# Performance work log

Hardware: AMD Instinct MI355X
Metric: run time of the kernel (lower is better)

The kernel has to match this reference:

```python
import jax, jax.numpy as jnp
import numpy as np

D_MODEL, H, D_K = 768, 12, 64
B, S = 2, 2048
NEG = -1.0e9


def setup_inputs() -> dict:
    key = jax.random.key(0)
    ks = jax.random.split(key, 7)
    q = jax.random.normal(ks[0], (B, S, D_MODEL), dtype=jnp.float32)
    k = jax.random.normal(ks[1], (B, S, D_MODEL), dtype=jnp.float32)
    v = jax.random.normal(ks[2], (B, S, D_MODEL), dtype=jnp.float32)
    mask = jnp.tril(jnp.ones((S, S), dtype=jnp.int32))[None, None]  # [1,1,S,S] causal
    sc = 1.0 / np.sqrt(D_MODEL)
    w_q = jax.random.normal(ks[3], (D_MODEL, D_MODEL), dtype=jnp.float32) * sc
    w_k = jax.random.normal(ks[4], (D_MODEL, D_MODEL), dtype=jnp.float32) * sc
    w_v = jax.random.normal(ks[5], (D_MODEL, D_MODEL), dtype=jnp.float32) * sc
    w_o = jax.random.normal(ks[6], (D_MODEL, D_MODEL), dtype=jnp.float32) * sc
    return {"q": q, "k": k, "v": v, "mask": mask,
            "w_q": w_q, "w_k": w_k, "w_v": w_v, "w_o": w_o}


def reference(q, k, v, mask, w_q, w_k, w_v, w_o):
    # nn.Linear(x) = x @ W.T ; split heads: [B,S,D] -> [B,H,S,Dk]
    def split_heads(x, w):
        y = jnp.einsum('bsd,ed->bse', x, w)
        return y.reshape(x.shape[0], x.shape[1], H, D_K).transpose(0, 2, 1, 3)

    qh = split_heads(q, w_q)
    kh = split_heads(k, w_k)
    vh = split_heads(v, w_v)
    scores = jnp.einsum('bhqd,bhkd->bhqk', qh, kh) / jnp.sqrt(jnp.float32(D_K))
    scores = jnp.where(mask == 0, jnp.float32(NEG), scores)
    attn = jax.nn.softmax(scores, axis=-1)  # dropout p=0 -> identity
    ctx = jnp.einsum('bhqk,bhkd->bhqd', attn, vh)
    ctx = ctx.transpose(0, 2, 1, 3).reshape(q.shape[0], q.shape[1], D_MODEL)
    return jnp.einsum('bsd,ed->bse', ctx, w_o)
```

## Files before the change

kernel.cpp:

```cpp
#include <hip/hip_runtime.h>

#define DM   768
#define HN   12
#define DKH  64
#define BSZ  2
#define SEQ  2048
#define MROWS (BSZ*SEQ)
#define NEGBIG -1.0e9f
#define NSLOT 40
#define QSCALE 0.18033688011112042f

typedef __bf16 bf16;
typedef __bf16 bf16x8 __attribute__((ext_vector_type(8)));
typedef __bf16 bf16x4 __attribute__((ext_vector_type(4)));
typedef float  f32x4  __attribute__((ext_vector_type(4)));
typedef unsigned int uint32;

__device__ __forceinline__ void gload_lds16(const void* g, void* l) {
    __builtin_amdgcn_global_load_lds(
        (const __attribute__((address_space(1))) char*)g,
        (__attribute__((address_space(3))) char*)l, 16, 0, 0);
}

__global__ __launch_bounds__(256) void cvt4(const float* __restrict__ a, const float* __restrict__ b,
                                            const float* __restrict__ c, const float* __restrict__ e,
                                            bf16* __restrict__ x, bf16* __restrict__ y,
                                            bf16* __restrict__ z, bf16* __restrict__ u, int n) {
    const float* s; bf16* d;
    if      (blockIdx.y == 0) { s = a; d = x; }
    else if (blockIdx.y == 1) { s = b; d = y; }
    else if (blockIdx.y == 2) { s = c; d = z; }
    else                      { s = e; d = u; }
    int i = (blockIdx.x * 256 + threadIdx.x) * 4;
    if (i + 3 < n) {
        float4 v = *(const float4*)(s + i);
        bf16x4 o; o[0] = (bf16)v.x; o[1] = (bf16)v.y; o[2] = (bf16)v.z; o[3] = (bf16)v.w;
        *(bf16x4*)(d + i) = o;
    }
}

__global__ __launch_bounds__(256) void gemm_qkv(
    const float* __restrict__ xq, const float* __restrict__ xk, const float* __restrict__ xv,
    const bf16* __restrict__ wq, const bf16* __restrict__ wk, const bf16* __restrict__ wv,
    bf16* __restrict__ qh, bf16* __restrict__ kh, bf16* __restrict__ vt)
{
    __shared__ float Asf[128 * 32];
    __shared__ bf16  Bs[128 * 32];

    const float* A; const bf16* Bw; bf16* Out; float qs;
    if      (blockIdx.z == 0) { A = xq; Bw = wq; Out = qh; qs = QSCALE; }
    else if (blockIdx.z == 1) { A = xk; Bw = wk; Out = kh; qs = 1.0f; }
    else                      { A = xv; Bw = wv; Out = vt; qs = 1.0f; }
    const bool vout = (blockIdx.z == 2);

    const int t = threadIdx.x, w = t >> 6, lane = t & 63;
    const int g = lane >> 4, lo = lane & 15;
    const int mt = blockIdx.x * 128, nt = blockIdx.y * 128;
    const int wr = (w >> 1) * 64, wc = (w & 1) * 64;

    f32x4 acc[4][4] = {};

    for (int k0 = 0; k0 < DM; k0 += 32) {
        #pragma unroll
        for (int i = 0; i < 4; i++) {
            int c = i * 256 + t;
            int row = c >> 3, cc = (c & 7) ^ (row & 7);
            gload_lds16(A + (size_t)(mt + row) * DM + k0 + cc * 4, (char*)Asf + c * 16);
        }
        #pragma unroll
        for (int i = 0; i < 2; i++) {
            int c = i * 256 + t;
            int row = c >> 2, col = (c & 3) * 8;
            gload_lds16(Bw + (size_t)(nt + row) * DM + k0 + col, (char*)Bs + c * 16);
        }
        asm volatile("s_waitcnt vmcnt(0)" ::: "memory");
        __syncthreads();

        bf16x8 af[4], bfr[4];
        #pragma unroll
        for (int m = 0; m < 4; m++) {
            int row = wr + m * 16 + lo;
            const char* rp = (const char*)Asf + row * 128;
            float4 f0 = *(const float4*)(rp + (((2 * g)     ^ (lo & 7)) << 4));
            float4 f1 = *(const float4*)(rp + (((2 * g + 1) ^ (lo & 7)) << 4));
            bf16x8 a;
            a[0] = (bf16)f0.x; a[1] = (bf16)f0.y; a[2] = (bf16)f0.z; a[3] = (bf16)f0.w;
            a[4] = (bf16)f1.x; a[5] = (bf16)f1.y; a[6] = (bf16)f1.z; a[7] = (bf16)f1.w;
            af[m] = a;
        }
        #pragma unroll
        for (int n = 0; n < 4; n++)
            bfr[n] = *(const bf16x8*)&Bs[(wc + n * 16 + lo) * 32 + g * 8];
        #pragma unroll
        for (int m = 0; m < 4; m++)
            #pragma unroll
            for (int n = 0; n < 4; n++)
                acc[m][n] = __builtin_amdgcn_mfma_f32_16x16x32_bf16(af[m], bfr[n], acc[m][n], 0, 0, 0);
        __syncthreads();
    }

    if (!vout) {
        #pragma unroll
        for (int m = 0; m < 4; m++) {
            #pragma unroll
            for (int n = 0; n < 4; n++) {
                #pragma unroll
                for (int r = 0; r < 4; r++) {
                    int gm = mt + wr + m * 16 + g * 4 + r;
                    int gn = nt + wc + n * 16 + lo;
                    int b = gm >> 11, s = gm & 2047, h = gn >> 6, d = gn & 63;
                    Out[(((size_t)b * HN + h) * SEQ + s) * DKH + d] = (bf16)(acc[m][n][r] * qs);
                }
            }
        }
    } else {
        #pragma unroll
        for (int m = 0; m < 4; m++) {
            #pragma unroll
            for (int n = 0; n < 4; n++) {
                int gm = mt + wr + m * 16 + g * 4;
                int gn = nt + wc + n * 16 + lo;
                int b = gm >> 11, s0 = gm & 2047, h = gn >> 6, d = gn & 63;
                bf16x4 pk;
                #pragma unroll
                for (int r = 0; r < 4; r++) pk[r] = (bf16)acc[m][n][r];
                *(bf16x4*)&Out[(((size_t)b * HN + h) * DKH + d) * SEQ + s0] = pk;
            }
        }
    }
}

__global__ __launch_bounds__(256) void gemm_out(
    const bf16* __restrict__ Actx, const bf16* __restrict__ Bw, float* __restrict__ Out)
{
    __shared__ bf16 As[128 * 32];
    __shared__ bf16 Bs[128 * 32];

    const int t = threadIdx.x, w = t >> 6, lane = t & 63;
    const int mt = blockIdx.x * 128, nt = blockIdx.y * 128;
    const int wr = (w >> 1) * 64, wc = (w & 1) * 64;

    f32x4 acc[4][4] = {};

    for (int k0 = 0; k0 < DM; k0 += 32) {
        #pragma unroll
        for (int i = 0; i < 2; i++) {
            int c = i * 256 + t;
            int row = c >> 2, col = (c & 3) * 8;
            gload_lds16(Actx + (size_t)(mt + row) * DM + k0 + col, (char*)As + c * 16);
            gload_lds16(Bw   + (size_t)(nt + row) * DM + k0 + col, (char*)Bs + c * 16);
        }
        asm volatile("s_waitcnt vmcnt(0)" ::: "memory");
        __syncthreads();

        bf16x8 af[4], bfr[4];
        #pragma unroll
        for (int m = 0; m < 4; m++)
            af[m] = *(const bf16x8*)&As[(wr + m * 16 + (lane & 15)) * 32 + (lane >> 4) * 8];
        #pragma unroll
        for (int n = 0; n < 4; n++)
            bfr[n] = *(const bf16x8*)&Bs[(wc + n * 16 + (lane & 15)) * 32 + (lane >> 4) * 8];
        #pragma unroll
        for (int m = 0; m < 4; m++)
            #pragma unroll
            for (int n = 0; n < 4; n++)
                acc[m][n] = __builtin_amdgcn_mfma_f32_16x16x32_bf16(af[m], bfr[n], acc[m][n], 0, 0, 0);
        __syncthreads();
    }

    #pragma unroll
    for (int m = 0; m < 4; m++) {
        #pragma unroll
        for (int n = 0; n < 4; n++) {
            #pragma unroll
            for (int r = 0; r < 4; r++) {
                int gm = mt + wr + m * 16 + (lane >> 4) * 4 + r;
                int gn = nt + wc + n * 16 + (lane & 15);
                Out[(size_t)gm * DM + gn] = acc[m][n][r];
            }
        }
    }
}

__global__ __launch_bounds__(256, 3) void flash_split(
    const bf16* __restrict__ qh, const bf16* __restrict__ kh,
    const bf16* __restrict__ vt, bf16* __restrict__ ctx,
    bf16* __restrict__ pO, float* __restrict__ pM, float* __restrict__ pL)
{
    __shared__ bf16 Ks[2][4096];
    __shared__ bf16 Vs[2][4096];
    __shared__ bf16 pl[4][1024];

    const int bid = blockIdx.x;
    const int slot = bid / 24;
    const int bh = bid % 24;

    int qt, p, np;
    if (slot < 16)      { qt = 15 - (slot >> 2); p = slot & 3;  np = 4; }
    else if (slot < 28) { int s = slot - 16; qt = 11 - s / 3; p = s % 3; np = 3; }
    else if (slot < 36) { int s = slot - 28; qt = 7 - (s >> 1); p = s & 1; np = 2; }
    else                { qt = 39 - slot; p = 0; np = 1; }

    const int T = 2 * qt + 2;
    const int bse = T / np, rem = T - bse * np;
    const int cnt   = bse + (p < rem ? 1 : 0);
    const int start = p * bse + (p < rem ? p : rem);

    const int qb = qt * 128;
    const int t = threadIdx.x, w = t >> 6, lane = t & 63;
    const int g = lane >> 4, lo = lane & 15;
    const size_t base = (size_t)bh * SEQ * DKH;
    const char* khead = (const char*)(kh + base);
    const char* vhead = (const char*)(vt + base);

    uint32 koff[2], voff[2];
    #pragma unroll
    for (int i = 0; i < 2; i++) {
        int c = w * 128 + i * 64 + lane;
        int r = c >> 3, s = c & 7;
        int sw = s ^ (r & 7);
        koff[i] = (uint32)(r * 128  + 16 * sw);
        voff[i] = (uint32)(r * 4096 + 16 * sw);
    }
    const uint32 kr0 = (uint32)(128 * lo + 16 * (g ^ (lo & 7)));
    const uint32 kr1 = kr0 ^ 64;

    uint32 pw[4], pr[2];
    #pragma unroll
    for (int cg = 0; cg < 4; cg++)
        pw[cg] = (uint32)(lo * 128 + (((2 * cg + (g >> 1)) ^ (lo & 7)) << 4) + (g & 1) * 8);
    #pragma unroll
    for (int kq = 0; kq < 2; kq++)
        pr[kq] = (uint32)(lo * 128 + (((4 * kq + g) ^ (lo & 7)) << 4));
    char* plb = (char*)&pl[w][0];

    const int qrow0 = qb + 16 * w + lo;
    const int qrow1 = qb + 64 + 16 * w + lo;
    const bf16* qp0 = qh + base + (size_t)qrow0 * DKH + g * 8;
    const bf16* qp1 = qh + base + (size_t)qrow1 * DKH + g * 8;
    bf16x8 qa0 = *(const bf16x8*)qp0;
    bf16x8 qa1 = *(const bf16x8*)(qp0 + 32);
    bf16x8 qb0 = *(const bf16x8*)qp1;
    bf16x8 qb1 = *(const bf16x8*)(qp1 + 32);

    f32x4 O0[4] = {}, O1[4] = {};
    float m0 = -1e30f, l0 = 0.0f, m1 = -1e30f, l1 = 0.0f;

    #pragma unroll
    for (int i = 0; i < 2; i++) {
        int c16 = (w * 128 + i * 64 + lane) * 16;
        gload_lds16(khead + (size_t)start * 8192 + koff[i], (char*)&Ks[0][0] + c16);
        gload_lds16(vhead + (size_t)start * 128  + voff[i], (char*)&Vs[0][0] + c16);
    }
    asm volatile("s_waitcnt vmcnt(0)" ::: "memory");
    __syncthreads();

    for (int it = 0; it < cnt; ++it) {
        const int kt = start + it;
        const int par = it & 1, nxt = par ^ 1;
        if (it + 1 < cnt) {
            const char* ks = khead + (size_t)(kt + 1) * 8192;
            const char* vs = vhead + (size_t)(kt + 1) * 128;
            #pragma unroll
            for (int i = 0; i < 2; i++) {
                int c16 = (w * 128 + i * 64 + lane) * 16;
                gload_lds16(ks + koff[i], (char*)&Ks[nxt][0] + c16);
                gload_lds16(vs + voff[i], (char*)&Vs[nxt][0] + c16);
            }
        }

        const bool act0  = (kt != T - 1);
        const bool diag0 = (kt == T - 2);
        const bool diag1 = (kt == T - 1);

        const char* Kp = (const char*)&Ks[par][0];
        f32x4 s0[4], s1[4];
        {
            bf16x8 kf0[4], kf1[4];
            #pragma unroll
            for (int cg = 0; cg < 4; cg++) {
                kf0[cg] = *(const bf16x8*)(Kp + cg * 2048 + kr0);
                kf1[cg] = *(const bf16x8*)(Kp + cg * 2048 + kr1);
            }
            __builtin_amdgcn_s_setprio(1);
            if (act0) {
                #pragma unroll
                for (int cg = 0; cg < 4; cg++) {
                    f32x4 z = {0.0f, 0.0f, 0.0f, 0.0f};
                    z = __builtin_amdgcn_mfma_f32_16x16x32_bf16(kf0[cg], qa0, z, 0, 0, 0);
                    z = __builtin_amdgcn_mfma_f32_16x16x32_bf16(kf1[cg], qa1, z, 0, 0, 0);
                    s0[cg] = z;
                }
            }
            #pragma unroll
            for (int cg = 0; cg < 4; cg++) {
                f32x4 z = {0.0f, 0.0f, 0.0f, 0.0f};
                z = __builtin_amdgcn_mfma_f32_16x16x32_bf16(kf0[cg], qb0, z, 0, 0, 0);
                z = __builtin_amdgcn_mfma_f32_16x16x32_bf16(kf1[cg], qb1, z, 0, 0, 0);
                s1[cg] = z;
            }
            __builtin_amdgcn_s_setprio(0);
        }

        if (act0 && diag0) {
            #pragma unroll
            for (int cg = 0; cg < 4; cg++)
                #pragma unroll
                for (int r = 0; r < 4; r++) {
                    int ki = kt * 64 + cg * 16 + 4 * g + r;
                    s0[cg][r] = (ki > qrow0) ? NEGBIG : s0[cg][r];
                }
        }
        if (diag1) {
            #pragma unroll
            for (int cg = 0; cg < 4; cg++)
                #pragma unroll
                for (int r = 0; r < 4; r++) {
                    int ki = kt * 64 + cg * 16 + 4 * g + r;
                    s1[cg][r] = (ki > qrow1) ? NEGBIG : s1[cg][r];
                }
        }

        if (act0) {
            float mx = fmaxf(fmaxf(fmaxf(s0[0][0], s0[0][1]), fmaxf(s0[0][2], s0[0][3])),
                             fmaxf(fmaxf(s0[1][0], s0[1][1]), fmaxf(s0[1][2], s0[1][3])));
            mx = fmaxf(mx, fmaxf(fmaxf(fmaxf(s0[2][0], s0[2][1]), fmaxf(s0[2][2], s0[2][3])),
                                 fmaxf(fmaxf(s0[3][0], s0[3][1]), fmaxf(s0[3][2], s0[3][3]))));
            mx = fmaxf(mx, __shfl_xor(mx, 16, 64));
            mx = fmaxf(mx, __shfl_xor(mx, 32, 64));
            if (!__all(mx - m0 <= 8.0f)) {
                float mnew = fmaxf(m0, mx);
                float scl = __builtin_exp2f(m0 - mnew);
                m0 = mnew; l0 *= scl;
                float s4[4];
                #pragma unroll
                for (int r = 0; r < 4; r++) s4[r] = __shfl(scl, 4 * g + r, 64);
                #pragma unroll
                for (int dg = 0; dg < 4; dg++)
                    #pragma unroll
                    for (int r = 0; r < 4; r++) O0[dg][r] *= s4[r];
            }
            float rs = 0.0f;
            #pragma unroll
            for (int cg = 0; cg < 4; cg++)
                #pragma unroll
                for (int r = 0; r < 4; r++) {
                    s0[cg][r] = __builtin_exp2f(s0[cg][r] - m0);
                    rs += s0[cg][r];
                }
            rs += __shfl_xor(rs, 16, 64);
            rs += __shfl_xor(rs, 32, 64);
            l0 += rs;
        }
        {
            float mx = fmaxf(fmaxf(fmaxf(s1[0][0], s1[0][1]), fmaxf(s1[0][2], s1[0][3])),
                             fmaxf(fmaxf(s1[1][0], s1[1][1]), fmaxf(s1[1][2], s1[1][3])));
            mx = fmaxf(mx, fmaxf(fmaxf(fmaxf(s1[2][0], s1[2][1]), fmaxf(s1[2][2], s1[2][3])),
                                 fmaxf(fmaxf(s1[3][0], s1[3][1]), fmaxf(s1[3][2], s1[3][3]))));
            mx = fmaxf(mx, __shfl_xor(mx, 16, 64));
            mx = fmaxf(mx, __shfl_xor(mx, 32, 64));
            if (!__all(mx - m1 <= 8.0f)) {
                float mnew = fmaxf(m1, mx);
                float scl = __builtin_exp2f(m1 - mnew);
                m1 = mnew; l1 *= scl;
                float s4[4];
                #pragma unroll
                for (int r = 0; r < 4; r++) s4[r] = __shfl(scl, 4 * g + r, 64);
                #pragma unroll
                for (int dg = 0; dg < 4; dg++)
                    #pragma unroll
                    for (int r = 0; r < 4; r++) O1[dg][r] *= s4[r];
            }
            float rs = 0.0f;
            #pragma unroll
            for (int cg = 0; cg < 4; cg++)
                #pragma unroll
                for (int r = 0; r < 4; r++) {
                    s1[cg][r] = __builtin_exp2f(s1[cg][r] - m1);
                    rs += s1[cg][r];
                }
            rs += __shfl_xor(rs, 16, 64);
            rs += __shfl_xor(rs, 32, 64);
            l1 += rs;
        }

        const char* Vp = (const char*)&Vs[par][0];
        bf16x8 vv[8];
        #pragma unroll
        for (int kq = 0; kq < 2; kq++)
            #pragma unroll
            for (int dblk = 0; dblk < 4; dblk++)
                vv[kq * 4 + dblk] = *(const bf16x8*)
                    (Vp + (dblk * 16 + lo) * 128 + 16 * ((4 * kq + g) ^ (lo & 7)));

        if (act0) {
            #pragma unroll
            for (int cg = 0; cg < 4; cg++) {
                bf16x4 pk;
                #pragma unroll
                for (int r = 0; r < 4; r++) pk[r] = (bf16)s0[cg][r];
                *(bf16x4*)(plb + pw[cg]) = pk;
            }
        }
        asm volatile("s_waitcnt lgkmcnt(0)" ::: "memory");
        __builtin_amdgcn_sched_barrier(0);
        if (act0) {
            __builtin_amdgcn_s_setprio(1);
            #pragma unroll
            for (int kq = 0; kq < 2; kq++) {
                bf16x8 pa = *(const bf16x8*)(plb + pr[kq]);
                #pragma unroll
                for (int dblk = 0; dblk < 4; dblk++)
                    O0[dblk] = __builtin_amdgcn_mfma_f32_16x16x32_bf16(pa, vv[kq * 4 + dblk], O0[dblk], 0, 0, 0);
            }
            __builtin_amdgcn_s_setprio(0);
        }
        __builtin_amdgcn_sched_barrier(0);
        {
            #pragma unroll
            for (int cg = 0; cg < 4; cg++) {
                bf16x4 pk;
                #pragma unroll
                for (int r = 0; r < 4; r++) pk[r] = (bf16)s1[cg][r];
                *(bf16x4*)(plb + pw[cg]) = pk;
            }
            asm volatile("s_waitcnt lgkmcnt(0)" ::: "memory");
            __builtin_amdgcn_sched_barrier(0);
            __builtin_amdgcn_s_setprio(1);
            #pragma unroll
            for (int kq = 0; kq < 2; kq++) {
                bf16x8 pa = *(const bf16x8*)(plb + pr[kq]);
                #pragma unroll
                for (int dblk = 0; dblk < 4; dblk++)
                    O1[dblk] = __builtin_amdgcn_mfma_f32_16x16x32_bf16(pa, vv[kq * 4 + dblk], O1[dblk], 0, 0, 0);
            }
            __builtin_amdgcn_s_setprio(0);
        }

        asm volatile("s_waitcnt vmcnt(0)" ::: "memory");
        __syncthreads();
    }

    if (np == 1) {
        const int b = bh / HN, h = bh % HN;
        float inv0[4], inv1[4];
        #pragma unroll
        for (int r = 0; r < 4; r++) {
            inv0[r] = 1.0f / __shfl(l0, 4 * g + r, 64);
            inv1[r] = 1.0f / __shfl(l1, 4 * g + r, 64);
        }
        #pragma unroll
        for (int dg = 0; dg < 4; dg++) {
            #pragma unroll
            for (int r = 0; r < 4; r++) {
                int row0 = qb + 16 * w + g * 4 + r;
                int row1 = qb + 64 + 16 * w + g * 4 + r;
                ctx[((size_t)(b * SEQ + row0)) * DM + h * DKH + dg * 16 + lo] =
                    (bf16)(O0[dg][r] * inv0[r]);
                ctx[((size_t)(b * SEQ + row1)) * DM + h * DKH + dg * 16 + lo] =
                    (bf16)(O1[dg][r] * inv1[r]);
            }
        }
    } else {
        const int pslot = bh * NSLOT + slot;
        bf16* po = pO + (size_t)pslot * 128 * 64;
        #pragma unroll
        for (int dg = 0; dg < 4; dg++) {
            #pragma unroll
            for (int r = 0; r < 4; r++) {
                int r0 = 16 * w + 4 * g + r;
                po[r0 * 64 + dg * 16 + lo]        = (bf16)O0[dg][r];
                po[(64 + r0) * 64 + dg * 16 + lo] = (bf16)O1[dg][r];
            }
        }
        if (g == 0) {
            pM[pslot * 128 + 16 * w + lo]      = m0;
            pL[pslot * 128 + 16 * w + lo]      = l0;
            pM[pslot * 128 + 64 + 16 * w + lo] = m1;
            pL[pslot * 128 + 64 + 16 * w + lo] = l1;
        }
    }
}

__global__ __launch_bounds__(256) void flash_combine(
    const bf16* __restrict__ pO, const float* __restrict__ pM,
    const float* __restrict__ pL, bf16* __restrict__ ctx)
{
    const int bh = blockIdx.x;
    const int qt = 4 + blockIdx.y;
    int np, s0;
    if (qt >= 12)     { np = 4; s0 = (15 - qt) * 4; }
    else if (qt >= 8) { np = 3; s0 = 16 + (11 - qt) * 3; }
    else              { np = 2; s0 = 28 + (7 - qt) * 2; }

    const int t = threadIdx.x;
    const int row = t >> 1, dh = (t & 1) * 32;
    const int pbase = bh * NSLOT + s0;

    float mi[4], wi[4];
    float mstar = -1e30f;
    #pragma unroll
    for (int i = 0; i < 4; i++)
        if (i < np) { mi[i] = pM[(pbase + i) * 128 + row]; mstar = fmaxf(mstar, mi[i]); }
    float lsum = 0.0f;
    #pragma unroll
    for (int i = 0; i < 4; i++)
        if (i < np) { wi[i] = __builtin_exp2f(mi[i] - mstar); lsum += wi[i] * pL[(pbase + i) * 128 + row]; }
    const float linv = 1.0f / lsum;

    const int b = bh / HN, h = bh % HN;
    bf16* crow = ctx + ((size_t)(b * SEQ + qt * 128 + row)) * DM + h * DKH + dh;

    #pragma unroll
    for (int d0 = 0; d0 < 32; d0 += 8) {
        float acc[8] = {};
        #pragma unroll
        for (int i = 0; i < 4; i++) {
            if (i < np) {
                bf16x8 o = *(const bf16x8*)&pO[((size_t)(pbase + i) * 128 + row) * 64 + dh + d0];
                #pragma unroll
                for (int j = 0; j < 8; j++) acc[j] += wi[i] * (float)o[j];
            }
        }
        bf16x8 ov;
        #pragma unroll
        for (int j = 0; j < 8; j++) ov[j] = (bf16)(acc[j] * linv);
        *(bf16x8*)(crow + d0) = ov;
    }
}

extern "C" void kernel_launch(void* const* d_in, const int* in_sizes, int n_in,
                              void* d_out, int out_size, void* d_ws, size_t ws_size,
                              hipStream_t stream) {
    const float* q  = (const float*)d_in[0];
    const float* k  = (const float*)d_in[1];
    const float* v  = (const float*)d_in[2];
    const float* wq = (const float*)d_in[4];
    const float* wk = (const float*)d_in[5];
    const float* wv = (const float*)d_in[6];
    const float* wo = (const float*)d_in[7];
    float* out = (float*)d_out;

    const size_t NX = (size_t)MROWS * DM;
    const size_t NW = (size_t)DM * DM;

    bf16* p = (bf16*)d_ws;
    bf16* wqb = p; p += NW;
    bf16* wkb = p; p += NW;
    bf16* wvb = p; p += NW;
    bf16* wob = p; p += NW;
    bf16* qhp = p; p += NX;
    bf16* khp = p; p += NX;
    bf16* vtp = p; p += NX;
    bf16* ctxp = p; p += NX;
    bf16* pO = p; p += (size_t)24 * NSLOT * 128 * 64;
    float* pM = (float*)p;
    float* pL = pM + 24 * NSLOT * 128;

    cvt4<<<dim3(NW / 1024, 4), 256, 0, stream>>>(wq, wk, wv, wo, wqb, wkb, wvb, wob, (int)NW);

    gemm_qkv<<<dim3(MROWS / 128, DM / 128, 3), 256, 0, stream>>>(
        q, k, v, wqb, wkb, wvb, qhp, khp, vtp);

    flash_split<<<24 * NSLOT, 256, 0, stream>>>(qhp, khp, vtp, ctxp, pO, pM, pL);
    flash_combine<<<dim3(24, 12), 256, 0, stream>>>(pO, pM, pL, ctxp);

    gemm_out<<<dim3(MROWS / 128, DM / 128), 256, 0, stream>>>(ctxp, wob, out);
}
```

Baseline: 104.5 us.

## Fuse split-KV combine into flash kernel via atomic counter; read fp32 W_o directly

The separate flash_combine launch is removed. Each split block now bumps an atomic counter per (head, query tile), and the last block to arrive merges the partial outputs using the max and sum statistics. Separately, gemm_out loads the fp32 output weight straight into an XOR-swizzled LDS tile and converts it to bf16 in registers, so W_o no longer needs its own conversion pass or bf16 buffer. This saves a kernel launch and the W_o conversion traffic, but adds a memset, atomics and fences, doubles B-tile LDS use, and puts conversion work in the gemm_out inner loop.

```diff
diff --git a/kernel.cpp b/kernel.cpp
--- a/kernel.cpp
+++ b/kernel.cpp
@@ -22,15 +22,14 @@
         (__attribute__((address_space(3))) char*)l, 16, 0, 0);
 }
 
-__global__ __launch_bounds__(256) void cvt4(const float* __restrict__ a, const float* __restrict__ b,
-                                            const float* __restrict__ c, const float* __restrict__ e,
+__global__ __launch_bounds__(256) void cvt3(const float* __restrict__ a, const float* __restrict__ b,
+                                            const float* __restrict__ c,
                                             bf16* __restrict__ x, bf16* __restrict__ y,
-                                            bf16* __restrict__ z, bf16* __restrict__ u, int n) {
+                                            bf16* __restrict__ z, int n) {
     const float* s; bf16* d;
     if      (blockIdx.y == 0) { s = a; d = x; }
     else if (blockIdx.y == 1) { s = b; d = y; }
-    else if (blockIdx.y == 2) { s = c; d = z; }
-    else                      { s = e; d = u; }
+    else                      { s = c; d = z; }
     int i = (blockIdx.x * 256 + threadIdx.x) * 4;
     if (i + 3 < n) {
         float4 v = *(const float4*)(s + i);
@@ -131,12 +130,13 @@
 }
 
 __global__ __launch_bounds__(256) void gemm_out(
-    const bf16* __restrict__ Actx, const bf16* __restrict__ Bw, float* __restrict__ Out)
+    const bf16* __restrict__ Actx, const float* __restrict__ Bw, float* __restrict__ Out)
 {
-    __shared__ bf16 As[128 * 32];
-    __shared__ bf16 Bs[128 * 32];
+    __shared__ bf16  As[128 * 32];
+    __shared__ float Bsf[128 * 32];
 
     const int t = threadIdx.x, w = t >> 6, lane = t & 63;
+    const int g = lane >> 4, lo = lane & 15;
     const int mt = blockIdx.x * 128, nt = blockIdx.y * 128;
     const int wr = (w >> 1) * 64, wc = (w & 1) * 64;
 
@@ -148,7 +148,12 @@
             int c = i * 256 + t;
             int row = c >> 2, col = (c & 3) * 8;
             gload_lds16(Actx + (size_t)(mt + row) * DM + k0 + col, (char*)As + c * 16);
-            gload_lds16(Bw   + (size_t)(nt + row) * DM + k0 + col, (char*)Bs + c * 16);
+        }
+        #pragma unroll
+        for (int i = 0; i < 4; i++) {
+            int c = i * 256 + t;
+            int row = c >> 3, cc = (c & 7) ^ (row & 7);
+            gload_lds16(Bw + (size_t)(nt + row) * DM + k0 + cc * 4, (char*)Bsf + c * 16);
         }
         asm volatile("s_waitcnt vmcnt(0)" ::: "memory");
         __syncthreads();
@@ -156,10 +161,17 @@
         bf16x8 af[4], bfr[4];
         #pragma unroll
         for (int m = 0; m < 4; m++)
-            af[m] = *(const bf16x8*)&As[(wr + m * 16 + (lane & 15)) * 32 + (lane >> 4) * 8];
-        #pragma unroll
-        for (int n = 0; n < 4; n++)
-            bfr[n] = *(const bf16x8*)&Bs[(wc + n * 16 + (lane & 15)) * 32 + (lane >> 4) * 8];
+            af[m] = *(const bf16x8*)&As[(wr + m * 16 + lo) * 32 + g * 8];
+        #pragma unroll
+        for (int n = 0; n < 4; n++) {
+            const char* rp = (const char*)Bsf + (wc + n * 16 + lo) * 128;
+            float4 f0 = *(const float4*)(rp + (((2 * g)     ^ (lo & 7)) << 4));
+            float4 f1 = *(const float4*)(rp + (((2 * g + 1) ^ (lo & 7)) << 4));
+            bf16x8 b;
+            b[0] = (bf16)f0.x; b[1] = (bf16)f0.y; b[2] = (bf16)f0.z; b[3] = (bf16)f0.w;
+            b[4] = (bf16)f1.x; b[5] = (bf16)f1.y; b[6] = (bf16)f1.z; b[7] = (bf16)f1.w;
+            bfr[n] = b;
+        }
         #pragma unroll
         for (int m = 0; m < 4; m++)
             #pragma unroll
@@ -174,8 +186,8 @@
         for (int n = 0; n < 4; n++) {
             #pragma unroll
             for (int r = 0; r < 4; r++) {
-                int gm = mt + wr + m * 16 + (lane >> 4) * 4 + r;
-                int gn = nt + wc + n * 16 + (lane & 15);
+                int gm = mt + wr + m * 16 + g * 4 + r;
+                int gn = nt + wc + n * 16 + lo;
                 Out[(size_t)gm * DM + gn] = acc[m][n][r];
             }
         }
@@ -185,11 +197,13 @@
 __global__ __launch_bounds__(256, 3) void flash_split(
     const bf16* __restrict__ qh, const bf16* __restrict__ kh,
     const bf16* __restrict__ vt, bf16* __restrict__ ctx,
-    bf16* __restrict__ pO, float* __restrict__ pM, float* __restrict__ pL)
+    bf16* __restrict__ pO, float* __restrict__ pM, float* __restrict__ pL,
+    unsigned int* __restrict__ pCnt)
 {
     __shared__ bf16 Ks[2][4096];
     __shared__ bf16 Vs[2][4096];
     __shared__ bf16 pl[4][1024];
+    __shared__ int lastFlag;
 
     const int bid = blockIdx.x;
     const int slot = bid / 24;
@@ -461,7 +475,10 @@
                     (bf16)(O1[dg][r] * inv1[r]);
             }
         }
-    } else {
+        return;
+    }
+
+    {
         const int pslot = bh * NSLOT + slot;
         bf16* po = pO + (size_t)pslot * 128 * 64;
         #pragma unroll
@@ -480,52 +497,51 @@
             pL[pslot * 128 + 64 + 16 * w + lo] = l1;
         }
     }
-}
-
-__global__ __launch_bounds__(256) void flash_combine(
-    const bf16* __restrict__ pO, const float* __restrict__ pM,
-    const float* __restrict__ pL, bf16* __restrict__ ctx)
-{
-    const int bh = blockIdx.x;
-    const int qt = 4 + blockIdx.y;
-    int np, s0;
-    if (qt >= 12)     { np = 4; s0 = (15 - qt) * 4; }
-    else if (qt >= 8) { np = 3; s0 = 16 + (11 - qt) * 3; }
-    else              { np = 2; s0 = 28 + (7 - qt) * 2; }
-
-    const int t = threadIdx.x;
-    const int row = t >> 1, dh = (t & 1) * 32;
-    const int pbase = bh * NSLOT + s0;
-
-    float mi[4], wi[4];
-    float mstar = -1e30f;
-    #pragma unroll
-    for (int i = 0; i < 4; i++)
-        if (i < np) { mi[i] = pM[(pbase + i) * 128 + row]; mstar = fmaxf(mstar, mi[i]); }
-    float lsum = 0.0f;
-    #pragma unroll
-    for (int i = 0; i < 4; i++)
-        if (i < np) { wi[i] = __builtin_exp2f(mi[i] - mstar); lsum += wi[i] * pL[(pbase + i) * 128 + row]; }
-    const float linv = 1.0f / lsum;
-
-    const int b = bh / HN, h = bh % HN;
-    bf16* crow = ctx + ((size_t)(b * SEQ + qt * 128 + row)) * DM + h * DKH + dh;
-
-    #pragma unroll
-    for (int d0 = 0; d0 < 32; d0 += 8) {
-        float acc[8] = {};
-        #pragma unroll
-        for (int i = 0; i < 4; i++) {
-            if (i < np) {
-                bf16x8 o = *(const bf16x8*)&pO[((size_t)(pbase + i) * 128 + row) * 64 + dh + d0];
-                #pragma unroll
-                for (int j = 0; j < 8; j++) acc[j] += wi[i] * (float)o[j];
-            }
-        }
-        bf16x8 ov;
-        #pragma unroll
-        for (int j = 0; j < 8; j++) ov[j] = (bf16)(acc[j] * linv);
-        *(bf16x8*)(crow + d0) = ov;
+
+    __threadfence();
+    if (t == 0) {
+        unsigned int old = atomicAdd(&pCnt[bh * 16 + qt], 1u);
+        lastFlag = (old == (unsigned int)(np - 1));
+    }
+    __syncthreads();
+    if (!lastFlag) return;
+    __threadfence();
+
+    {
+        const int s0l = slot - p;
+        const int row = t >> 1, dh = (t & 1) * 32;
+        const int pbase = bh * NSLOT + s0l;
+
+        float mi[4], wi[4];
+        float mstar = -1e30f;
+        #pragma unroll
+        for (int i = 0; i < 4; i++)
+            if (i < np) { mi[i] = pM[(pbase + i) * 128 + row]; mstar = fmaxf(mstar, mi[i]); }
+        float lsum = 0.0f;
+        #pragma unroll
+        for (int i = 0; i < 4; i++)
+            if (i < np) { wi[i] = __builtin_exp2f(mi[i] - mstar); lsum += wi[i] * pL[(pbase + i) * 128 + row]; }
+        const float linv = 1.0f / lsum;
+
+        const int b = bh / HN, h = bh % HN;
+        bf16* crow = ctx + ((size_t)(b * SEQ + qb + row)) * DM + h * DKH + dh;
+
+        #pragma unroll
+        for (int d0 = 0; d0 < 32; d0 += 8) {
+            float acc[8] = {};
+            #pragma unroll
+            for (int i = 0; i < 4; i++) {
+                if (i < np) {
+                    bf16x8 o = *(const bf16x8*)&pO[((size_t)(pbase + i) * 128 + row) * 64 + dh + d0];
+                    #pragma unroll
+                    for (int j = 0; j < 8; j++) acc[j] += wi[i] * (float)o[j];
+                }
+            }
+            bf16x8 ov;
+            #pragma unroll
+            for (int j = 0; j < 8; j++) ov[j] = (bf16)(acc[j] * linv);
+            *(bf16x8*)(crow + d0) = ov;
+        }
     }
 }
 
@@ -548,7 +564,6 @@
     bf16* wqb = p; p += NW;
     bf16* wkb = p; p += NW;
     bf16* wvb = p; p += NW;
-    bf16* wob = p; p += NW;
     bf16* qhp = p; p += NX;
     bf16* khp = p; p += NX;
     bf16* vtp = p; p += NX;
@@ -556,14 +571,16 @@
     bf16* pO = p; p += (size_t)24 * NSLOT * 128 * 64;
     float* pM = (float*)p;
     float* pL = pM + 24 * NSLOT * 128;
-
-    cvt4<<<dim3(NW / 1024, 4), 256, 0, stream>>>(wq, wk, wv, wo, wqb, wkb, wvb, wob, (int)NW);
+    unsigned int* pCnt = (unsigned int*)(pL + 24 * NSLOT * 128);
+
+    hipMemsetAsync(pCnt, 0, 24 * 16 * sizeof(unsigned int), stream);
+
+    cvt3<<<dim3(NW / 1024, 3), 256, 0, stream>>>(wq, wk, wv, wqb, wkb, wvb, (int)NW);
 
     gemm_qkv<<<dim3(MROWS / 128, DM / 128, 3), 256, 0, stream>>>(
         q, k, v, wqb, wkb, wvb, qhp, khp, vtp);
 
-    flash_split<<<24 * NSLOT, 256, 0, stream>>>(qhp, khp, vtp, ctxp, pO, pM, pL);
-    flash_combine<<<dim3(24, 12), 256, 0, stream>>>(pO, pM, pL, ctxp);
-
-    gemm_out<<<dim3(MROWS / 128, DM / 128), 256, 0, stream>>>(ctxp, wob, out);
+    flash_split<<<24 * NSLOT, 256, 0, stream>>>(qhp, khp, vtp, ctxp, pO, pM, pL, pCnt);
+
+    gemm_out<<<dim3(MROWS / 128, DM / 128), 256, 0, stream>>>(ctxp, wo, out);
 }
```

Result: slower. 251.6 us (+140.7%).
